# Kernel optimization log

Hardware: AMD Instinct MI355X
Metric: run time of the kernel (lower is better)

Reference implementation:

```python
import jax, jax.numpy as jnp
import numpy as np

RC = 6.0            # cosine cutoff radius (Angstrom)
N_ANGULAR = 128     # module init arg; output dim = 3*N_ANGULAR
EPS = 1e-12


def cosine_cutoff(d):
    # Behler-style cosine cutoff: 0.5*(cos(pi*d/rc)+1) for d < rc, else 0
    return jnp.where(d < RC, 0.5 * (jnp.cos(jnp.pi * d / RC) + 1.0), 0.0)


def setup_inputs() -> dict:
    key = jax.random.key(0)
    k1, k2, k3, k4 = jax.random.split(key, 4)
    B, N, M = 8, 4096, 96
    L = 20.0  # box length
    positions = jax.random.uniform(k1, (B, N, 3), dtype=jnp.float32) * L
    cell = jnp.tile(jnp.eye(3, dtype=jnp.float32) * L, (B, 1, 1))
    neighbors = jax.random.randint(k2, (B, N, M), 0, N, dtype=jnp.int32)
    offsets = jax.random.randint(k3, (B, N, M, 3), -1, 2).astype(jnp.float32)
    mask = (jax.random.uniform(k4, (B, N, M)) > 0.1).astype(jnp.float32)
    return {"positions": positions, "cell": cell, "offsets": offsets,
            "mask": mask, "neighbors": neighbors}


def reference(positions, cell, offsets, mask, neighbors):
    B, N, M = neighbors.shape
    # gather neighbor positions: pos_j[b,n,m,:] = positions[b, neighbors[b,n,m], :]
    idx = neighbors.reshape(B, N * M)
    pos_j = jnp.take_along_axis(positions, idx[:, :, None], axis=1).reshape(B, N, M, 3)
    # displacement vectors with periodic offsets (offsets in cell coordinates)
    dis_vec = pos_j - positions[:, :, None, :] + jnp.einsum('bnmi,bij->bnmj', offsets, cell)
    distances = jnp.sqrt(jnp.sum(dis_vec * dis_vec, axis=-1) + EPS)  # [B,N,M]
    # cutoff / distance, zeroed where mask == 0
    cut = jnp.where(mask != 0.0, cosine_cutoff(distances) / distances, 0.0)
    # sort neighbors by descending cut value, gather cut-weighted vectors in that order
    order = jnp.argsort(-cut, axis=-1)                       # [B,N,M]
    cut_vec = cut[..., None] * dis_vec                       # [B,N,M,3]
    cut_vec = jnp.take_along_axis(cut_vec, order[..., None], axis=2)
    cut_vec = cut_vec.reshape(B, N, M * 3)
    # scatter into zero-padded descriptor of width 3*n_angular
    f = jnp.zeros((B, N, N_ANGULAR * 3), dtype=positions.dtype)
    f = f.at[:, :, : M * 3].set(cut_vec)
    return f
```

## Files before the change

### kernel.cpp

```cpp
#include <hip/hip_runtime.h>
#include <math.h>

#define M_NB   96
#define OUT_W  384
#define NATOM  4096
#define WPB    16
#define NITER  4

__device__ __forceinline__ void merge3(float4& a4, float2& a2, int base,
                                       float v0, float v1, float v2, int lane)
{
    const int f4lo = 4 * lane;
    const int f2lo = 256 + 2 * lane;
    const float v[3] = {v0, v1, v2};
    #pragma unroll
    for (int t = 0; t < 3; ++t) {
        const int idx = base + t;
        if      (idx == f4lo)     a4.x = v[t];
        else if (idx == f4lo + 1) a4.y = v[t];
        else if (idx == f4lo + 2) a4.z = v[t];
        else if (idx == f4lo + 3) a4.w = v[t];
        else if (idx == f2lo)     a2.x = v[t];
        else if (idx == f2lo + 1) a2.y = v[t];
    }
}

__global__ __launch_bounds__(64 * WPB, 8) void deepmd_angular_kernel(
    const float* __restrict__ positions,
    const float* __restrict__ cell,
    const float* __restrict__ offsets,
    const float* __restrict__ mask,
    const int*   __restrict__ neighbors,
    float*       __restrict__ out,
    int N)
{
    __shared__ float4 pos4_s[NATOM];
    __shared__ float  cut_s[WPB][M_NB];

    const int tid  = threadIdx.x;
    const int wv   = tid >> 6;
    const int lane = tid & 63;
    const bool low = lane < 32;

    const int p0 = blockIdx.x * (WPB * NITER);
    const int b  = p0 / N;

    {
        const float* pb_ = positions + (size_t)b * N * 3;
        for (int a = tid; a < NATOM; a += 64 * WPB) {
            const float3 v = *(const float3*)(pb_ + 3 * a);
            pos4_s[a] = make_float4(v.x, v.y, v.z, 0.f);
        }
    }
    __syncthreads();

    const float* cb = cell + (size_t)b * 9;
    const float c00 = cb[0], c01 = cb[1], c02 = cb[2];
    const float c10 = cb[3], c11 = cb[4], c12 = cb[5];
    const float c20 = cb[6], c21 = cb[7], c22 = cb[8];

    #pragma unroll
    for (int it = 0; it < NITER; ++it) {
        const int q  = p0 + wv * NITER + it;
        const int nn = q - b * N;

        const long eA = (long)q * M_NB + lane;
        const int    jA = neighbors[eA];
        const float mkA = mask[eA];
        const float3 oA = *(const float3*)(offsets + eA * 3);

        int jB = 0; float mkB = 0.f; float3 oB = make_float3(0.f, 0.f, 0.f);
        if (low) {
            const long eB = eA + 64;
            jB  = neighbors[eB];
            mkB = mask[eB];
            oB  = *(const float3*)(offsets + eB * 3);
        }

        const float4 pi  = pos4_s[nn];
        const float4 pjA = pos4_s[jA];

        const float dxA = pjA.x - pi.x + oA.x * c00 + oA.y * c10 + oA.z * c20;
        const float dyA = pjA.y - pi.y + oA.x * c01 + oA.y * c11 + oA.z * c21;
        const float dzA = pjA.z - pi.z + oA.x * c02 + oA.y * c12 + oA.z * c22;
        const float dA  = sqrtf(dxA * dxA + dyA * dyA + dzA * dzA + 1e-12f);
        float cutA = 0.f;
        if (mkA != 0.f && dA < 6.f)
            cutA = 0.5f * (cosf(dA * 0.52359877559829887f) + 1.f) / dA;

        float dxB = 0.f, dyB = 0.f, dzB = 0.f, cutB = 0.f;
        if (low) {
            const float4 pjB = pos4_s[jB];
            dxB = pjB.x - pi.x + oB.x * c00 + oB.y * c10 + oB.z * c20;
            dyB = pjB.y - pi.y + oB.x * c01 + oB.y * c11 + oB.z * c21;
            dzB = pjB.z - pi.z + oB.x * c02 + oB.y * c12 + oB.z * c22;
            const float dB = sqrtf(dxB * dxB + dyB * dyB + dzB * dzB + 1e-12f);
            if (mkB != 0.f && dB < 6.f)
                cutB = 0.5f * (cosf(dB * 0.52359877559829887f) + 1.f) / dB;
        }

        cut_s[wv][lane] = cutA;
        if (low) cut_s[wv][64 + lane] = cutB;

        int rkA = 0; float w0A = 0.f, w1A = 0.f, w2A = 0.f;
        if (cutA != 0.f) {
            const int mA = lane;
            int rank = 0;
            const float4* c4 = (const float4*)cut_s[wv];
            #pragma unroll
            for (int k4 = 0; k4 < M_NB / 4; ++k4) {
                const float4 c = c4[k4];
                const int k = 4 * k4;
                rank += (c.x > cutA) || (c.x == cutA && k + 0 < mA);
                rank += (c.y > cutA) || (c.y == cutA && k + 1 < mA);
                rank += (c.z > cutA) || (c.z == cutA && k + 2 < mA);
                rank += (c.w > cutA) || (c.w == cutA && k + 3 < mA);
            }
            rkA = rank; w0A = cutA * dxA; w1A = cutA * dyA; w2A = cutA * dzA;
        }
        int rkB = 0; float w0B = 0.f, w1B = 0.f, w2B = 0.f;
        if (low && cutB != 0.f) {
            const int mB = 64 + lane;
            int rank = 0;
            const float4* c4 = (const float4*)cut_s[wv];
            #pragma unroll
            for (int k4 = 0; k4 < M_NB / 4; ++k4) {
                const float4 c = c4[k4];
                const int k = 4 * k4;
                rank += (c.x > cutB) || (c.x == cutB && k + 0 < mB);
                rank += (c.y > cutB) || (c.y == cutB && k + 1 < mB);
                rank += (c.z > cutB) || (c.z == cutB && k + 2 < mB);
                rank += (c.w > cutB) || (c.w == cutB && k + 3 < mB);
            }
            rkB = rank; w0B = cutB * dxB; w1B = cutB * dyB; w2B = cutB * dzB;
        }

        unsigned long long bmA = __ballot(cutA != 0.f);
        unsigned long long bmB = __ballot(low && cutB != 0.f);
        float4 a4 = make_float4(0.f, 0.f, 0.f, 0.f);
        float2 a2 = make_float2(0.f, 0.f);
        while (bmA) {
            const int src = (int)__builtin_ctzll(bmA); bmA &= bmA - 1;
            const int   r  = __shfl(rkA, src);
            const float v0 = __shfl(w0A, src);
            const float v1 = __shfl(w1A, src);
            const float v2 = __shfl(w2A, src);
            merge3(a4, a2, 3 * r, v0, v1, v2, lane);
        }
        while (bmB) {
            const int src = (int)__builtin_ctzll(bmB); bmB &= bmB - 1;
            const int   r  = __shfl(rkB, src);
            const float v0 = __shfl(w0B, src);
            const float v1 = __shfl(w1B, src);
            const float v2 = __shfl(w2B, src);
            merge3(a4, a2, 3 * r, v0, v1, v2, lane);
        }

        float* rowp = out + (size_t)q * OUT_W;
        ((float4*)rowp)[lane] = a4;
        ((float2*)(rowp + 256))[lane] = a2;
    }
}

extern "C" void kernel_launch(void* const* d_in, const int* in_sizes, int n_in,
                              void* d_out, int out_size, void* d_ws, size_t ws_size,
                              hipStream_t stream) {
    const float* positions = (const float*)d_in[0];
    const float* cell      = (const float*)d_in[1];
    const float* offsets   = (const float*)d_in[2];
    const float* mask      = (const float*)d_in[3];
    const int*   neighbors = (const int*)d_in[4];
    float*       out       = (float*)d_out;

    const int BN = in_sizes[0] / 3;
    const int B  = in_sizes[1] / 9;
    const int N  = BN / B;

    dim3 block(64 * WPB, 1, 1);
    dim3 grid(BN / (WPB * NITER), 1, 1);
    deepmd_angular_kernel<<<grid, block, 0, stream>>>(
        positions, cell, offsets, mask, neighbors, out, N);
}
```

Measured before the change: 123.1 us.

## Compute neighbor ranks via wave ballots instead of shared-memory comparison loop

Replaces the per-lane O(M) rank computation over a shared-memory cut array with a per-source ballot/popcount rank computed inside the scatter loop, removing the cut_s LDS buffer and its 24 float4 reads per lane. Also switches cosf to the fast __cosf intrinsic. The ballot approach adds 3-4 ballots per nonzero neighbor in the serialized loop, and __cosf reduces accuracy slightly, which could perturb ordering of near-equal cut values.

New measurement: 118.4 us. 1.04x faster.

```diff
diff --git a/kernel.cpp b/kernel.cpp
--- a/kernel.cpp
+++ b/kernel.cpp
@@ -35,7 +35,6 @@
     int N)
 {
     __shared__ float4 pos4_s[NATOM];
-    __shared__ float  cut_s[WPB][M_NB];
 
     const int tid  = threadIdx.x;
     const int wv   = tid >> 6;
@@ -86,7 +85,7 @@
         const float dA  = sqrtf(dxA * dxA + dyA * dyA + dzA * dzA + 1e-12f);
         float cutA = 0.f;
         if (mkA != 0.f && dA < 6.f)
-            cutA = 0.5f * (cosf(dA * 0.52359877559829887f) + 1.f) / dA;
+            cutA = 0.5f * (__cosf(dA * 0.52359877559829887f) + 1.f) / dA;
 
         float dxB = 0.f, dyB = 0.f, dzB = 0.f, cutB = 0.f;
         if (low) {
@@ -96,64 +95,39 @@
             dzB = pjB.z - pi.z + oB.x * c02 + oB.y * c12 + oB.z * c22;
             const float dB = sqrtf(dxB * dxB + dyB * dyB + dzB * dzB + 1e-12f);
             if (mkB != 0.f && dB < 6.f)
-                cutB = 0.5f * (cosf(dB * 0.52359877559829887f) + 1.f) / dB;
+                cutB = 0.5f * (__cosf(dB * 0.52359877559829887f) + 1.f) / dB;
         }
 
-        cut_s[wv][lane] = cutA;
-        if (low) cut_s[wv][64 + lane] = cutB;
+        const float w0A = cutA * dxA, w1A = cutA * dyA, w2A = cutA * dzA;
+        const float w0B = cutB * dxB, w1B = cutB * dyB, w2B = cutB * dzB;
 
-        int rkA = 0; float w0A = 0.f, w1A = 0.f, w2A = 0.f;
-        if (cutA != 0.f) {
-            const int mA = lane;
-            int rank = 0;
-            const float4* c4 = (const float4*)cut_s[wv];
-            #pragma unroll
-            for (int k4 = 0; k4 < M_NB / 4; ++k4) {
-                const float4 c = c4[k4];
-                const int k = 4 * k4;
-                rank += (c.x > cutA) || (c.x == cutA && k + 0 < mA);
-                rank += (c.y > cutA) || (c.y == cutA && k + 1 < mA);
-                rank += (c.z > cutA) || (c.z == cutA && k + 2 < mA);
-                rank += (c.w > cutA) || (c.w == cutA && k + 3 < mA);
-            }
-            rkA = rank; w0A = cutA * dxA; w1A = cutA * dyA; w2A = cutA * dzA;
-        }
-        int rkB = 0; float w0B = 0.f, w1B = 0.f, w2B = 0.f;
-        if (low && cutB != 0.f) {
-            const int mB = 64 + lane;
-            int rank = 0;
-            const float4* c4 = (const float4*)cut_s[wv];
-            #pragma unroll
-            for (int k4 = 0; k4 < M_NB / 4; ++k4) {
-                const float4 c = c4[k4];
-                const int k = 4 * k4;
-                rank += (c.x > cutB) || (c.x == cutB && k + 0 < mB);
-                rank += (c.y > cutB) || (c.y == cutB && k + 1 < mB);
-                rank += (c.z > cutB) || (c.z == cutB && k + 2 < mB);
-                rank += (c.w > cutB) || (c.w == cutB && k + 3 < mB);
-            }
-            rkB = rank; w0B = cutB * dxB; w1B = cutB * dyB; w2B = cutB * dzB;
-        }
-
-        unsigned long long bmA = __ballot(cutA != 0.f);
-        unsigned long long bmB = __ballot(low && cutB != 0.f);
         float4 a4 = make_float4(0.f, 0.f, 0.f, 0.f);
         float2 a2 = make_float2(0.f, 0.f);
-        while (bmA) {
-            const int src = (int)__builtin_ctzll(bmA); bmA &= bmA - 1;
-            const int   r  = __shfl(rkA, src);
-            const float v0 = __shfl(w0A, src);
-            const float v1 = __shfl(w1A, src);
-            const float v2 = __shfl(w2A, src);
-            merge3(a4, a2, 3 * r, v0, v1, v2, lane);
+
+        unsigned long long t = __ballot(cutA != 0.f);
+        while (t) {
+            const int s = (int)__builtin_ctzll(t); t &= t - 1;
+            const float c = __shfl(cutA, s);
+            const unsigned long long gtA = __ballot(cutA > c);
+            const unsigned long long gtB = __ballot(cutB > c);
+            const unsigned long long eqA = __ballot(cutA == c);
+            const int rank = __popcll(gtA) + __popcll(gtB)
+                           + __popcll(eqA & ((1ull << s) - 1ull));
+            merge3(a4, a2, 3 * rank,
+                   __shfl(w0A, s), __shfl(w1A, s), __shfl(w2A, s), lane);
         }
-        while (bmB) {
-            const int src = (int)__builtin_ctzll(bmB); bmB &= bmB - 1;
-            const int   r  = __shfl(rkB, src);
-            const float v0 = __shfl(w0B, src);
-            const float v1 = __shfl(w1B, src);
-            const float v2 = __shfl(w2B, src);
-            merge3(a4, a2, 3 * r, v0, v1, v2, lane);
+        t = __ballot(cutB != 0.f);
+        while (t) {
+            const int s = (int)__builtin_ctzll(t); t &= t - 1;
+            const float c = __shfl(cutB, s);
+            const unsigned long long gtA = __ballot(cutA > c);
+            const unsigned long long gtB = __ballot(cutB > c);
+            const unsigned long long eqA = __ballot(cutA == c);
+            const unsigned long long eqB = __ballot(cutB == c);
+            const int rank = __popcll(gtA) + __popcll(gtB) + __popcll(eqA)
+                           + __popcll(eqB & ((1ull << s) - 1ull));
+            merge3(a4, a2, 3 * rank,
+                   __shfl(w0B, s), __shfl(w1B, s), __shfl(w2B, s), lane);
         }
 
         float* rowp = out + (size_t)q * OUT_W;
```
